# Optimization experiments

Measured on AMD Instinct MI355X. Metric: run time of the kernel, lower is better.

Reference implementation:

```python
import jax, jax.numpy as jnp
import numpy as np
from numpy.polynomial import Polynomial

B, C = 2000000, 10
EXP = dict(start=0.0, stop=1.0, n=1000, deg=8)
INV = dict(start=10.0, stop=30.0, n=1000, deg=4)
LOG = dict(start=0.01, stop=0.5, n=1000, deg=8)
ITERATIONS = 3


def _fit(fn, start, stop, n, deg):
    x = np.linspace(start, stop, n)
    return Polynomial.fit(x, fn(x), deg).convert(kind=Polynomial).coef.astype(np.float32)


def _polyval(coeffs, x):
    # Horner; coeffs ascending order (numpy Polynomial convention)
    res = jnp.full_like(x, coeffs[-1])
    for i in range(coeffs.shape[0] - 2, -1, -1):
        res = res * x + coeffs[i]
    return res


def setup_inputs() -> dict:
    key = jax.random.key(0)
    k1, k2 = jax.random.split(key)
    enc_input = jax.random.uniform(k1, (B, C), dtype=jnp.float32)  # logits in [0,1)
    labels = jax.random.randint(k2, (B,), 0, C)
    enc_target = jax.nn.one_hot(labels, C, dtype=jnp.float32)
    exp_coeffs = jnp.asarray(_fit(np.exp, **{'start': EXP['start'], 'stop': EXP['stop'], 'n': EXP['n'], 'deg': EXP['deg']}))
    inverse_coeffs = jnp.asarray(_fit(lambda x: 1.0 / x, INV['start'], INV['stop'], INV['n'], INV['deg']))
    log_coeffs = jnp.asarray(_fit(np.log, LOG['start'], LOG['stop'], LOG['n'], LOG['deg']))
    return {
        'enc_input': enc_input,
        'enc_target': enc_target,
        'exp_coeffs': exp_coeffs,
        'inverse_coeffs': inverse_coeffs,
        'log_coeffs': log_coeffs,
        'iterations': ITERATIONS,
    }


def reference(enc_input, enc_target, exp_coeffs, inverse_coeffs, log_coeffs, iterations):
    # exp via polynomial approximation (Horner / ciphertext poly eval)
    e = _polyval(exp_coeffs, enc_input)                      # [B, C]
    s = jnp.sum(e, axis=1, keepdims=True)                    # [B, 1]
    # inverse via polynomial initial guess + Newton-Raphson refinement
    inv = _polyval(inverse_coeffs, s)
    for _ in range(iterations):
        inv = inv * (2.0 - s * inv)
    softmax = e * inv                                        # [B, C]
    log_softmax = _polyval(log_coeffs, softmax)              # [B, C]
    # mean cross-entropy over the batch
    loss = -jnp.sum(enc_target * log_softmax) / enc_input.shape[0]
    return loss


if __name__ == '__main__':
    out = reference(**setup_inputs())
    print(out)
```

## Files before the change

### kernel.cpp

```cpp
#include <hip/hip_runtime.h>

#define CCOL 10

__global__ void zero_kernel(float* out) {
    if (threadIdx.x == 0 && blockIdx.x == 0) out[0] = 0.0f;
}

__global__ __launch_bounds__(256) void ce_kernel(
    const float* __restrict__ x, const float* __restrict__ tgt,
    const float* __restrict__ exp_c, const float* __restrict__ inv_c,
    const float* __restrict__ log_c, const int* __restrict__ iters_p,
    float* __restrict__ out, int npairs, float neg_inv_b)
{
    float ec[9], ic[5], lc[9];
#pragma unroll
    for (int i = 0; i < 9; i++) ec[i] = exp_c[i];
#pragma unroll
    for (int i = 0; i < 5; i++) ic[i] = inv_c[i];
#pragma unroll
    for (int i = 0; i < 9; i++) lc[i] = log_c[i];
    const int niter = iters_p[0];

    int tid = blockIdx.x * blockDim.x + threadIdx.x;
    float local = 0.0f;

    if (tid < npairs) {
        const float4* xv = (const float4*)(x   + (size_t)tid * (2 * CCOL));
        const float4* tv = (const float4*)(tgt + (size_t)tid * (2 * CCOL));
        float xr[2 * CCOL], tr[2 * CCOL];
#pragma unroll
        for (int i = 0; i < 5; i++) {
            float4 v = xv[i];
            xr[4 * i + 0] = v.x; xr[4 * i + 1] = v.y;
            xr[4 * i + 2] = v.z; xr[4 * i + 3] = v.w;
        }
#pragma unroll
        for (int i = 0; i < 5; i++) {
            float4 w = tv[i];
            tr[4 * i + 0] = w.x; tr[4 * i + 1] = w.y;
            tr[4 * i + 2] = w.z; tr[4 * i + 3] = w.w;
        }

#pragma unroll
        for (int r = 0; r < 2; r++) {
            float e[CCOL];
            float s = 0.0f;
#pragma unroll
            for (int c = 0; c < CCOL; c++) {
                float xx = xr[r * CCOL + c];
                float v = ec[8];
#pragma unroll
                for (int i = 7; i >= 0; i--) v = fmaf(v, xx, ec[i]);
                e[c] = v;
                s += v;
            }
            float inv = ic[4];
#pragma unroll
            for (int i = 3; i >= 0; i--) inv = fmaf(inv, s, ic[i]);
            for (int k = 0; k < niter; k++) inv = inv * (2.0f - s * inv);

#pragma unroll
            for (int c = 0; c < CCOL; c++) {
                float sm = e[c] * inv;
                float v = lc[8];
#pragma unroll
                for (int i = 7; i >= 0; i--) v = fmaf(v, sm, lc[i]);
                local = fmaf(tr[r * CCOL + c], v, local);
            }
        }
    }

#pragma unroll
    for (int off = 32; off > 0; off >>= 1)
        local += __shfl_down(local, off, 64);

    __shared__ float wsum[4];
    int lane = threadIdx.x & 63;
    int wid  = threadIdx.x >> 6;
    if (lane == 0) wsum[wid] = local;
    __syncthreads();
    if (threadIdx.x == 0) {
        float b = wsum[0] + wsum[1] + wsum[2] + wsum[3];
        atomicAdd(out, b * neg_inv_b);
    }
}

extern "C" void kernel_launch(void* const* d_in, const int* in_sizes, int n_in,
                              void* d_out, int out_size, void* d_ws, size_t ws_size,
                              hipStream_t stream) {
    const float* x  = (const float*)d_in[0];
    const float* t  = (const float*)d_in[1];
    const float* ec = (const float*)d_in[2];
    const float* ic = (const float*)d_in[3];
    const float* lc = (const float*)d_in[4];
    const int*   it = (const int*)d_in[5];
    float* out = (float*)d_out;

    int b_rows = in_sizes[0] / CCOL;
    int npairs = b_rows / 2;
    float neg_inv_b = -1.0f / (float)b_rows;

    zero_kernel<<<1, 64, 0, stream>>>(out);

    const int threads = 256;
    int blocks = (npairs + threads - 1) / threads;
    ce_kernel<<<blocks, threads, 0, stream>>>(x, t, ec, ic, lc, it, out,
                                              npairs, neg_inv_b);
}
```

Measured before the change: 188.7 us.

## Stage input tiles into LDS via direct global-to-LDS loads

Full blocks now load their input and target tiles with coalesced per-wave 16-byte global_load_lds transfers into shared memory, then each thread reads its pair from LDS. The tail block keeps the old direct float4 path. This aims to improve global access coalescing, but costs 40 KB of LDS per block (lower occupancy) and an extra barrier.

```diff
diff --git a/kernel.cpp b/kernel.cpp
--- a/kernel.cpp
+++ b/kernel.cpp
@@ -1,17 +1,27 @@
 #include <hip/hip_runtime.h>
 
 #define CCOL 10
+#define TPB 256
+#define PAIR_BYTES 80
+#define WAVE_BYTES (64 * PAIR_BYTES)
+#define CHUNK 1024
+
+typedef const __attribute__((address_space(1))) void* gptr_t;
+typedef __attribute__((address_space(3))) void* lptr_t;
 
 __global__ void zero_kernel(float* out) {
     if (threadIdx.x == 0 && blockIdx.x == 0) out[0] = 0.0f;
 }
 
-__global__ __launch_bounds__(256) void ce_kernel(
+__global__ __launch_bounds__(TPB) void ce_kernel(
     const float* __restrict__ x, const float* __restrict__ tgt,
     const float* __restrict__ exp_c, const float* __restrict__ inv_c,
     const float* __restrict__ log_c, const int* __restrict__ iters_p,
-    float* __restrict__ out, int npairs, float neg_inv_b)
+    float* __restrict__ out, int npairs, int full_blocks, float neg_inv_b)
 {
+    __shared__ float sx[TPB * 2 * CCOL];
+    __shared__ float st[TPB * 2 * CCOL];
+
     float ec[9], ic[5], lc[9];
 #pragma unroll
     for (int i = 0; i < 9; i++) ec[i] = exp_c[i];
@@ -21,13 +31,29 @@
     for (int i = 0; i < 9; i++) lc[i] = log_c[i];
     const int niter = iters_p[0];
 
-    int tid = blockIdx.x * blockDim.x + threadIdx.x;
-    float local = 0.0f;
+    const int tid  = threadIdx.x;
+    const int lane = tid & 63;
+    const int w    = tid >> 6;
+    const int pair0 = blockIdx.x * TPB;
 
-    if (tid < npairs) {
-        const float4* xv = (const float4*)(x   + (size_t)tid * (2 * CCOL));
-        const float4* tv = (const float4*)(tgt + (size_t)tid * (2 * CCOL));
-        float xr[2 * CCOL], tr[2 * CCOL];
+    float xr[2 * CCOL], tr[2 * CCOL];
+    bool have = false;
+
+    if (blockIdx.x < full_blocks) {
+        const char* gx = (const char*)x   + (size_t)pair0 * PAIR_BYTES + w * WAVE_BYTES + lane * 16;
+        const char* gt = (const char*)tgt + (size_t)pair0 * PAIR_BYTES + w * WAVE_BYTES + lane * 16;
+        char* lx = (char*)sx + w * WAVE_BYTES + lane * 16;
+        char* lt = (char*)st + w * WAVE_BYTES + lane * 16;
+#pragma unroll
+        for (int i = 0; i < 5; i++)
+            __builtin_amdgcn_global_load_lds((gptr_t)(gx + i * CHUNK), (lptr_t)(lx + i * CHUNK), 16, 0, 0);
+#pragma unroll
+        for (int i = 0; i < 5; i++)
+            __builtin_amdgcn_global_load_lds((gptr_t)(gt + i * CHUNK), (lptr_t)(lt + i * CHUNK), 16, 0, 0);
+        __syncthreads();
+
+        const float4* xv = (const float4*)(sx + tid * 2 * CCOL);
+        const float4* tv = (const float4*)(st + tid * 2 * CCOL);
 #pragma unroll
         for (int i = 0; i < 5; i++) {
             float4 v = xv[i];
@@ -36,11 +62,34 @@
         }
 #pragma unroll
         for (int i = 0; i < 5; i++) {
-            float4 w = tv[i];
-            tr[4 * i + 0] = w.x; tr[4 * i + 1] = w.y;
-            tr[4 * i + 2] = w.z; tr[4 * i + 3] = w.w;
+            float4 v = tv[i];
+            tr[4 * i + 0] = v.x; tr[4 * i + 1] = v.y;
+            tr[4 * i + 2] = v.z; tr[4 * i + 3] = v.w;
         }
+        have = true;
+    } else {
+        int p = pair0 + tid;
+        if (p < npairs) {
+            const float4* xv = (const float4*)(x   + (size_t)p * 2 * CCOL);
+            const float4* tv = (const float4*)(tgt + (size_t)p * 2 * CCOL);
+#pragma unroll
+            for (int i = 0; i < 5; i++) {
+                float4 v = xv[i];
+                xr[4 * i + 0] = v.x; xr[4 * i + 1] = v.y;
+                xr[4 * i + 2] = v.z; xr[4 * i + 3] = v.w;
+            }
+#pragma unroll
+            for (int i = 0; i < 5; i++) {
+                float4 v = tv[i];
+                tr[4 * i + 0] = v.x; tr[4 * i + 1] = v.y;
+                tr[4 * i + 2] = v.z; tr[4 * i + 3] = v.w;
+            }
+            have = true;
+        }
+    }
 
+    float local = 0.0f;
+    if (have) {
 #pragma unroll
         for (int r = 0; r < 2; r++) {
             float e[CCOL];
@@ -75,11 +124,9 @@
         local += __shfl_down(local, off, 64);
 
     __shared__ float wsum[4];
-    int lane = threadIdx.x & 63;
-    int wid  = threadIdx.x >> 6;
-    if (lane == 0) wsum[wid] = local;
+    if (lane == 0) wsum[w] = local;
     __syncthreads();
-    if (threadIdx.x == 0) {
+    if (tid == 0) {
         float b = wsum[0] + wsum[1] + wsum[2] + wsum[3];
         atomicAdd(out, b * neg_inv_b);
     }
@@ -100,10 +147,11 @@
     int npairs = b_rows / 2;
     float neg_inv_b = -1.0f / (float)b_rows;
 
+    int full_blocks = npairs / TPB;
+    int tail = npairs - full_blocks * TPB;
+    int blocks = full_blocks + (tail ? 1 : 0);
+
     zero_kernel<<<1, 64, 0, stream>>>(out);
-
-    const int threads = 256;
-    int blocks = (npairs + threads - 1) / threads;
-    ce_kernel<<<blocks, threads, 0, stream>>>(x, t, ec, ic, lc, it, out,
-                                              npairs, neg_inv_b);
+    ce_kernel<<<blocks, TPB, 0, stream>>>(x, t, ec, ic, lc, it, out,
+                                          npairs, full_blocks, neg_inv_b);
 }
```

Result: no change. 190.6 us (+1.0%).
